# Optimization experiments

Measured on AMD Instinct MI355X. Metric: run time of the kernel, lower is better.

The kernel has to match this reference:

```python
import jax, jax.numpy as jnp
import numpy as np

N_HEADS = 16


def setup_inputs() -> dict:
    key = jax.random.key(0)
    ks = jax.random.split(key, 5)
    B, T, C = 4, 2048, 1024
    scale = 0.02
    return {
        "x": jax.random.normal(ks[0], (B, T, C), dtype=jnp.float32),
        "w_attn": jax.random.normal(ks[1], (C, 3 * C), dtype=jnp.float32) * scale,
        "b_attn": jax.random.normal(ks[2], (3 * C,), dtype=jnp.float32) * scale,
        "w_proj": jax.random.normal(ks[3], (C, C), dtype=jnp.float32) * scale,
        "b_proj": jax.random.normal(ks[4], (C,), dtype=jnp.float32) * scale,
    }


def reference(x, w_attn, b_attn, w_proj, b_proj):
    B, T, C = x.shape
    H = N_HEADS
    D = C // H  # head dim
    qkv = x @ w_attn + b_attn  # [B,T,3C]
    q, k, v = jnp.split(qkv, 3, axis=-1)
    # [B,T,C] -> [B,H,T,D]
    q = q.reshape(B, T, H, D).transpose(0, 2, 1, 3)
    k = k.reshape(B, T, H, D).transpose(0, 2, 1, 3)
    v = v.reshape(B, T, H, D).transpose(0, 2, 1, 3)
    att = jnp.einsum("bhtd,bhsd->bhts", q, k) * (1.0 / jnp.sqrt(jnp.float32(D)))
    causal = jnp.tril(jnp.ones((T, T), dtype=bool))  # [T,T]
    att = jnp.where(causal[None, None], att, -jnp.inf)
    att = jax.nn.softmax(att, axis=-1)
    y = jnp.einsum("bhts,bhsd->bhtd", att, v)  # [B,H,T,D]
    y = y.transpose(0, 2, 1, 3).reshape(B, T, C)
    return y @ w_proj + b_proj
```

## Files before the change

### kernel.cpp

```cpp
#include <hip/hip_runtime.h>
#include <hip/hip_bf16.h>
#include <math.h>

typedef __attribute__((ext_vector_type(8))) short short8;
typedef __attribute__((ext_vector_type(4))) short short4v;
typedef __attribute__((ext_vector_type(4))) float f32x4;
typedef __attribute__((ext_vector_type(2))) unsigned int uint2v;
typedef unsigned int u32;

#define MFMA16(a, b, c) __builtin_amdgcn_mfma_f32_16x16x16bf16_1k(a, b, c, 0, 0, 0)
#define MFMA32(a, b, c) __builtin_amdgcn_mfma_f32_16x16x32_bf16(a, b, c, 0, 0, 0)

#define GLB(p) ((const __attribute__((address_space(1))) u32*)(p))
#define LDS(p) ((__attribute__((address_space(3))) u32*)(p))

#define QSCALE 0.18033688011111204f

#define KV_STRIDE 72
#define KV_TILE 4608
#define KV_CHUNK 9216

__device__ __forceinline__ unsigned short f2bf(float f) {
  unsigned int u = __float_as_uint(f);
  u += 0x7fffu + ((u >> 16) & 1u);
  return (unsigned short)(u >> 16);
}


__global__ __launch_bounds__(256) void cvt_bf16(const float* __restrict__ in,
                                                unsigned short* __restrict__ out, int n4) {
  int i = blockIdx.x * blockDim.x + threadIdx.x;
  if (i < n4) {
    float4 f = ((const float4*)in)[i];
    ushort4 o;
    o.x = f2bf(f.x); o.y = f2bf(f.y); o.z = f2bf(f.z); o.w = f2bf(f.w);
    ((ushort4*)out)[i] = o;
  }
}

__global__ __launch_bounds__(256) void transpose_cvt(const float* __restrict__ in,
                                                     unsigned short* __restrict__ out,
                                                     int R, int C) {
  __shared__ float tile[32][33];
  int bx = blockIdx.x * 32;
  int by = blockIdx.y * 32;
  int tx = threadIdx.x, ty = threadIdx.y;
#pragma unroll
  for (int i = 0; i < 32; i += 8)
    tile[ty + i][tx] = in[(size_t)(by + ty + i) * C + bx + tx];
  __syncthreads();
#pragma unroll
  for (int i = 0; i < 32; i += 8)
    out[(size_t)(bx + ty + i) * R + by + tx] = f2bf(tile[tx][ty + i]);
}


template <int MODE>
__global__ __launch_bounds__(256)
void gemm_bt(const unsigned short* __restrict__ A, const unsigned short* __restrict__ Bt,
             const float* __restrict__ bias, float* __restrict__ outf,
             unsigned short* __restrict__ q_ws, unsigned short* __restrict__ kv_ws,
             int M, int N, int K) {
  __shared__ unsigned short As[128 * 32];
  __shared__ unsigned short Bs[128 * 32];
  const int tid = threadIdx.x;
  const int wid = tid >> 6;
  const int lane = tid & 63;
  const int quad = lane >> 4;
  const int l15 = lane & 15;
  const int m0 = blockIdx.x * 128;
  const int n0 = blockIdx.y * 128;
  const int wm = (wid >> 1) * 64;
  const int wn = (wid & 1) * 64;

  const int srow = wid * 32 + (lane >> 2);
  const int scol = (lane & 3) * 8;
  const unsigned short* ga0 = A + (size_t)(m0 + srow) * K + scol;
  const unsigned short* ga1 = ga0 + (size_t)16 * K;
  const unsigned short* gb0 = Bt + (size_t)(n0 + srow) * K + scol;
  const unsigned short* gb1 = gb0 + (size_t)16 * K;
  unsigned short* la0 = As + srow * 32 + scol;
  unsigned short* la1 = la0 + 16 * 32;
  unsigned short* lb0 = Bs + srow * 32 + scol;
  unsigned short* lb1 = lb0 + 16 * 32;

  f32x4 acc[4][4];
#pragma unroll
  for (int i = 0; i < 4; i++)
#pragma unroll
    for (int j = 0; j < 4; j++) acc[i][j] = (f32x4){0.f, 0.f, 0.f, 0.f};

  for (int k0 = 0; k0 < K; k0 += 32) {
    __builtin_amdgcn_global_load_lds(GLB(ga0 + k0), LDS(la0), 16, 0, 0);
    __builtin_amdgcn_global_load_lds(GLB(ga1 + k0), LDS(la1), 16, 0, 0);
    __builtin_amdgcn_global_load_lds(GLB(gb0 + k0), LDS(lb0), 16, 0, 0);
    __builtin_amdgcn_global_load_lds(GLB(gb1 + k0), LDS(lb1), 16, 0, 0);
    __syncthreads();
    short8 af[4], bf[4];
#pragma unroll
    for (int i = 0; i < 4; i++)
      af[i] = *(const short8*)(As + (wm + i * 16 + l15) * 32 + quad * 8);
#pragma unroll
    for (int j = 0; j < 4; j++)
      bf[j] = *(const short8*)(Bs + (wn + j * 16 + l15) * 32 + quad * 8);
#pragma unroll
    for (int i = 0; i < 4; i++)
#pragma unroll
      for (int j = 0; j < 4; j++)
        acc[i][j] = MFMA32(af[i], bf[j], acc[i][j]);
    __syncthreads();
  }

  const int colbase = n0 + wn;
  const int which = colbase >> 10;

  if (MODE == 0 && which == 2) {
    short4v idf;
#pragma unroll
    for (int j4 = 0; j4 < 4; j4++) idf[j4] = (quad * 4 + j4 == l15) ? (short)0x3F80 : (short)0;
    const int cb = colbase & 1023;
    const int h = cb >> 6;
#pragma unroll
    for (int j = 0; j < 4; j++) {
      const float bv = bias[colbase + j * 16 + l15];
      const int d0 = (cb & 63) + j * 16 + quad * 4;
#pragma unroll
      for (int i = 0; i < 4; i++) {
        short4v pf;
#pragma unroll
        for (int r = 0; r < 4; r++) pf[r] = (short)f2bf(acc[i][j][r] + bv);
        f32x4 dt = MFMA16(pf, idf, ((f32x4){0.f, 0.f, 0.f, 0.f}));
        const int t = m0 + wm + i * 16 + l15;
        const int b = t >> 11;
        const int tt = t & 2047;
        const size_t cbase =
            ((size_t)((b * 16 + h) * 32) + (tt >> 6)) * KV_CHUNK + KV_TILE;
        const int tl = tt & 63;
#pragma unroll
        for (int r = 0; r < 4; r++)
          kv_ws[cbase + (size_t)(d0 + r) * KV_STRIDE + tl] = f2bf(dt[r]);
      }
    }
  } else {
#pragma unroll
    for (int j = 0; j < 4; j++) {
      const int col = colbase + j * 16 + l15;
      const float bv = bias[col];
#pragma unroll
      for (int i = 0; i < 4; i++) {
#pragma unroll
        for (int r = 0; r < 4; r++) {
          const int row = m0 + wm + i * 16 + quad * 4 + r;
          float v = acc[i][j][r] + bv;
          if (MODE == 0) {
            const int c = col & 1023;
            const int h = c >> 6;
            const int d = c & 63;
            const int b = row >> 11;
            const int t = row & 2047;
            if (which == 0) {
              q_ws[(((size_t)(b * 16 + h) * 2048 + t) * 64) + d] = f2bf(v * QSCALE);
            } else {
              const size_t cbase = ((size_t)((b * 16 + h) * 32) + (t >> 6)) * KV_CHUNK;
              kv_ws[cbase + (size_t)(t & 63) * KV_STRIDE + d] = f2bf(v);
            }
          } else {
            outf[(size_t)row * N + col] = v;
          }
        }
      }
    }
  }
}


__global__ __launch_bounds__(256, 4)
void attn_fwd(const unsigned short* __restrict__ q_ws, const unsigned short* __restrict__ kv_ws,
              unsigned short* __restrict__ y_ws) {
  __shared__ unsigned short KV[2][KV_CHUNK];
  const int tid = threadIdx.x;
  const int w = tid >> 6;
  const int lane = tid & 63;
  const int quad = lane >> 4;
  const int l15 = lane & 15;
  const int ip = blockIdx.x;
  const int bh = blockIdx.y;
  const unsigned short* Qp = q_ws + (size_t)bh * 2048 * 64;
  const unsigned short* KVp = kv_ws + (size_t)bh * 32 * KV_CHUNK;

  const int qA = ip * 64 + w * 16;
  const int qB = (31 - ip) * 64 + w * 16;

  short8 qfr[2][2];
#pragma unroll
  for (int c = 0; c < 2; c++) {
    qfr[0][c] = *(const short8*)(Qp + (size_t)(qA + l15) * 64 + c * 32 + quad * 8);
    qfr[1][c] = *(const short8*)(Qp + (size_t)(qB + l15) * 64 + c * 32 + quad * 8);
  }

  f32x4 o[2][4];
#pragma unroll
  for (int f = 0; f < 2; f++)
#pragma unroll
    for (int db = 0; db < 4; db++) o[f][db] = (f32x4){0.f, 0.f, 0.f, 0.f};
  float lsum[2] = {0.f, 0.f};

  const int nch = 32 - ip;

  for (int i = w; i < 18; i += 4)
    __builtin_amdgcn_global_load_lds(GLB(KVp + i * 512 + lane * 8),
                                     LDS(&KV[0][i * 512 + lane * 8]), 16, 0, 0);

  for (int c = 0; c < nch; c++) {
    __syncthreads();
    const int buf = c & 1;
    if (c + 1 < nch) {
      const unsigned short* src = KVp + (size_t)(c + 1) * KV_CHUNK;
      for (int i = w; i < 18; i += 4)
        __builtin_amdgcn_global_load_lds(GLB(src + i * 512 + lane * 8),
                                         LDS(&KV[buf ^ 1][i * 512 + lane * 8]), 16, 0, 0);
    }
    const unsigned short* Ksb = KV[buf];
    const unsigned short* Vtb = KV[buf] + KV_TILE;
    const int kbase = c * 64;

#pragma unroll
    for (int tb = 0; tb < 2; tb++) {
      const int kb = kbase + tb * 32;
      if (kb > qB + 15) break;
      const int kloc = tb * 32;
      short8 kf[2][2];
#pragma unroll
      for (int t2 = 0; t2 < 2; t2++)
#pragma unroll
        for (int cc = 0; cc < 2; cc++)
          kf[t2][cc] =
              *(const short8*)(&Ksb[(kloc + t2 * 16 + l15) * KV_STRIDE + cc * 32 + quad * 8]);
      short4v vf[2][4];
#pragma unroll
      for (int t2 = 0; t2 < 2; t2++)
#pragma unroll
        for (int db = 0; db < 4; db++)
          vf[t2][db] =
              *(const short4v*)(&Vtb[(db * 16 + l15) * KV_STRIDE + kloc + t2 * 16 + quad * 4]);

#pragma unroll
      for (int f = 0; f < 2; f++) {
        const int qf0 = f ? qB : qA;
        if (kb > qf0 + 15) continue;
        f32x4 s0 = (f32x4){0.f, 0.f, 0.f, 0.f};
        f32x4 s1 = (f32x4){0.f, 0.f, 0.f, 0.f};
        s0 = MFMA32(kf[0][0], qfr[f][0], s0);
        s0 = MFMA32(kf[0][1], qfr[f][1], s0);
        s1 = MFMA32(kf[1][0], qfr[f][0], s1);
        s1 = MFMA32(kf[1][1], qfr[f][1], s1);
        const int qg = qf0 + l15;
        if (kb + 31 > qf0) {
#pragma unroll
          for (int r = 0; r < 4; r++) {
            if (kb + quad * 4 + r > qg) s0[r] = -INFINITY;
            if (kb + 16 + quad * 4 + r > qg) s1[r] = -INFINITY;
          }
        }
        float p[8];
#pragma unroll
        for (int r = 0; r < 4; r++) {
          p[r] = __builtin_amdgcn_exp2f(s0[r]);
          p[4 + r] = __builtin_amdgcn_exp2f(s1[r]);
        }
        lsum[f] += ((p[0] + p[1]) + (p[2] + p[3])) + ((p[4] + p[5]) + (p[6] + p[7]));
        u32 u[8];
#pragma unroll
        for (int i = 0; i < 8; i++) u[i] = __float_as_uint(p[i]) + 0x8000u;
        uint2v t0, t1;
        t0.x = __builtin_amdgcn_perm(u[1], u[0], 0x07060302u);
        t0.y = __builtin_amdgcn_perm(u[3], u[2], 0x07060302u);
        t1.x = __builtin_amdgcn_perm(u[5], u[4], 0x07060302u);
        t1.y = __builtin_amdgcn_perm(u[7], u[6], 0x07060302u);
        short4v pf0 = __builtin_bit_cast(short4v, t0);
        short4v pf1 = __builtin_bit_cast(short4v, t1);
#pragma unroll
        for (int db = 0; db < 4; db++) {
          o[f][db] = MFMA16(vf[0][db], pf0, o[f][db]);
          o[f][db] = MFMA16(vf[1][db], pf1, o[f][db]);
        }
      }
    }
  }

  const int b = bh >> 4, h = bh & 15;
#pragma unroll
  for (int f = 0; f < 2; f++) {
    float ls = lsum[f];
    ls += __shfl_xor(ls, 16);
    ls += __shfl_xor(ls, 32);
    const int qg = (f ? qB : qA) + l15;
    const float inv = 1.0f / ls;
    const size_t rowoff = ((size_t)(b * 2048 + qg)) * 1024 + h * 64;
#pragma unroll
    for (int db = 0; db < 4; db++) {
      ushort4 ov;
      ov.x = f2bf(o[f][db][0] * inv);
      ov.y = f2bf(o[f][db][1] * inv);
      ov.z = f2bf(o[f][db][2] * inv);
      ov.w = f2bf(o[f][db][3] * inv);
      *(ushort4*)(y_ws + rowoff + db * 16 + quad * 4) = ov;
    }
  }
}


extern "C" void kernel_launch(void* const* d_in, const int* in_sizes, int n_in,
                              void* d_out, int out_size, void* d_ws, size_t ws_size,
                              hipStream_t stream) {
  const float* x = (const float*)d_in[0];
  const float* w_attn = (const float*)d_in[1];
  const float* b_attn = (const float*)d_in[2];
  const float* w_proj = (const float*)d_in[3];
  const float* b_proj = (const float*)d_in[4];
  float* out = (float*)d_out;

  unsigned short* xb = (unsigned short*)d_ws;
  unsigned short* wat = xb + (size_t)8192 * 1024;
  unsigned short* wpt = wat + (size_t)3072 * 1024;
  unsigned short* q_ws = wpt + (size_t)1024 * 1024;
  unsigned short* kv_ws = q_ws + (size_t)8388608;
  unsigned short* y_ws = xb;

  cvt_bf16<<<8192, 256, 0, stream>>>(x, xb, 2097152);
  transpose_cvt<<<dim3(96, 32), dim3(32, 8), 0, stream>>>(w_attn, wat, 1024, 3072);
  transpose_cvt<<<dim3(32, 32), dim3(32, 8), 0, stream>>>(w_proj, wpt, 1024, 1024);

  gemm_bt<0><<<dim3(64, 24), 256, 0, stream>>>(xb, wat, b_attn, nullptr, q_ws, kv_ws,
                                               8192, 3072, 1024);
  attn_fwd<<<dim3(16, 64), 256, 0, stream>>>(q_ws, kv_ws, y_ws);
  gemm_bt<1><<<dim3(64, 8), 256, 0, stream>>>(y_ws, wpt, b_proj, out, nullptr, nullptr,
                                              8192, 1024, 1024);
}
```

Before: 272.6 us.

## Process four query tiles per attention block and vectorize QKV epilogue stores

Each attention block now handles four balanced query tiles (ip, 15-ip, 16+ip, 31-ip) instead of two, halving the grid. Each KV chunk staged in LDS is therefore reused by twice as many query fragments, which cuts global and LDS loading per unit of work. The cost is more accumulator registers per thread, the removal of the occupancy hint from the launch bounds, and fewer blocks to spread across CUs. Separately, the QKV GEMM epilogue writes Q and K through the MFMA identity-transpose trick and writes V directly, all as 4-wide ushort4 stores instead of scalar stores.

```diff
diff --git a/kernel.cpp b/kernel.cpp
--- a/kernel.cpp
+++ b/kernel.cpp
@@ -114,31 +114,62 @@
   const int colbase = n0 + wn;
   const int which = colbase >> 10;
 
-  if (MODE == 0 && which == 2) {
-    short4v idf;
-#pragma unroll
-    for (int j4 = 0; j4 < 4; j4++) idf[j4] = (quad * 4 + j4 == l15) ? (short)0x3F80 : (short)0;
-    const int cb = colbase & 1023;
-    const int h = cb >> 6;
-#pragma unroll
-    for (int j = 0; j < 4; j++) {
-      const float bv = bias[colbase + j * 16 + l15];
-      const int d0 = (cb & 63) + j * 16 + quad * 4;
-#pragma unroll
-      for (int i = 0; i < 4; i++) {
-        short4v pf;
-#pragma unroll
-        for (int r = 0; r < 4; r++) pf[r] = (short)f2bf(acc[i][j][r] + bv);
-        f32x4 dt = MFMA16(pf, idf, ((f32x4){0.f, 0.f, 0.f, 0.f}));
-        const int t = m0 + wm + i * 16 + l15;
-        const int b = t >> 11;
-        const int tt = t & 2047;
-        const size_t cbase =
-            ((size_t)((b * 16 + h) * 32) + (tt >> 6)) * KV_CHUNK + KV_TILE;
-        const int tl = tt & 63;
-#pragma unroll
-        for (int r = 0; r < 4; r++)
-          kv_ws[cbase + (size_t)(d0 + r) * KV_STRIDE + tl] = f2bf(dt[r]);
+  if (MODE == 0) {
+    const int h = (colbase & 1023) >> 6;
+    if (which == 2) {
+#pragma unroll
+      for (int j = 0; j < 4; j++) {
+        const float bv = bias[colbase + j * 16 + l15];
+        const int d = j * 16 + l15;
+#pragma unroll
+        for (int i = 0; i < 4; i++) {
+          const int t = m0 + wm + i * 16 + quad * 4;
+          const int b = t >> 11;
+          const int tt = t & 2047;
+          ushort4 pv;
+          pv.x = f2bf(acc[i][j][0] + bv);
+          pv.y = f2bf(acc[i][j][1] + bv);
+          pv.z = f2bf(acc[i][j][2] + bv);
+          pv.w = f2bf(acc[i][j][3] + bv);
+          const size_t cbase = ((size_t)((b * 16 + h) * 32) + (tt >> 6)) * KV_CHUNK + KV_TILE;
+          *(ushort4*)(&kv_ws[cbase + (size_t)d * KV_STRIDE + (tt & 63)]) = pv;
+        }
+      }
+    } else {
+      short4v idf;
+#pragma unroll
+      for (int j4 = 0; j4 < 4; j4++)
+        idf[j4] = (quad * 4 + j4 == l15) ? (short)0x3F80 : (short)0;
+#pragma unroll
+      for (int j = 0; j < 4; j++) {
+        const float bv = bias[colbase + j * 16 + l15];
+#pragma unroll
+        for (int i = 0; i < 4; i++) {
+          short4v pf;
+          if (which == 0) {
+#pragma unroll
+            for (int r = 0; r < 4; r++) pf[r] = (short)f2bf((acc[i][j][r] + bv) * QSCALE);
+          } else {
+#pragma unroll
+            for (int r = 0; r < 4; r++) pf[r] = (short)f2bf(acc[i][j][r] + bv);
+          }
+          f32x4 dt = MFMA16(pf, idf, ((f32x4){0.f, 0.f, 0.f, 0.f}));
+          const int t = m0 + wm + i * 16 + l15;
+          const int b = t >> 11;
+          const int tt = t & 2047;
+          const int dd = j * 16 + quad * 4;
+          ushort4 qv;
+          qv.x = f2bf(dt[0]);
+          qv.y = f2bf(dt[1]);
+          qv.z = f2bf(dt[2]);
+          qv.w = f2bf(dt[3]);
+          if (which == 0) {
+            *(ushort4*)(&q_ws[(((size_t)((b * 16 + h) * 2048) + tt) * 64) + dd]) = qv;
+          } else {
+            const size_t cbase = ((size_t)((b * 16 + h) * 32) + (tt >> 6)) * KV_CHUNK;
+            *(ushort4*)(&kv_ws[cbase + (size_t)(tt & 63) * KV_STRIDE + dd]) = qv;
+          }
+        }
       }
     }
   } else {
@@ -151,22 +182,7 @@
 #pragma unroll
         for (int r = 0; r < 4; r++) {
           const int row = m0 + wm + i * 16 + quad * 4 + r;
-          float v = acc[i][j][r] + bv;
-          if (MODE == 0) {
-            const int c = col & 1023;
-            const int h = c >> 6;
-            const int d = c & 63;
-            const int b = row >> 11;
-            const int t = row & 2047;
-            if (which == 0) {
-              q_ws[(((size_t)(b * 16 + h) * 2048 + t) * 64) + d] = f2bf(v * QSCALE);
-            } else {
-              const size_t cbase = ((size_t)((b * 16 + h) * 32) + (t >> 6)) * KV_CHUNK;
-              kv_ws[cbase + (size_t)(t & 63) * KV_STRIDE + d] = f2bf(v);
-            }
-          } else {
-            outf[(size_t)row * N + col] = v;
-          }
+          outf[(size_t)row * N + col] = acc[i][j][r] + bv;
         }
       }
     }
@@ -174,7 +190,7 @@
 }
 
 
-__global__ __launch_bounds__(256, 4)
+__global__ __launch_bounds__(256)
 void attn_fwd(const unsigned short* __restrict__ q_ws, const unsigned short* __restrict__ kv_ws,
               unsigned short* __restrict__ y_ws) {
   __shared__ unsigned short KV[2][KV_CHUNK];
@@ -188,22 +204,25 @@
   const unsigned short* Qp = q_ws + (size_t)bh * 2048 * 64;
   const unsigned short* KVp = kv_ws + (size_t)bh * 32 * KV_CHUNK;
 
-  const int qA = ip * 64 + w * 16;
-  const int qB = (31 - ip) * 64 + w * 16;
-
-  short8 qfr[2][2];
-#pragma unroll
-  for (int c = 0; c < 2; c++) {
-    qfr[0][c] = *(const short8*)(Qp + (size_t)(qA + l15) * 64 + c * 32 + quad * 8);
-    qfr[1][c] = *(const short8*)(Qp + (size_t)(qB + l15) * 64 + c * 32 + quad * 8);
-  }
-
-  f32x4 o[2][4];
-#pragma unroll
-  for (int f = 0; f < 2; f++)
+  int qT[4];
+  qT[0] = ip * 64 + w * 16;
+  qT[1] = (15 - ip) * 64 + w * 16;
+  qT[2] = (16 + ip) * 64 + w * 16;
+  qT[3] = (31 - ip) * 64 + w * 16;
+
+  short8 qfr[4][2];
+#pragma unroll
+  for (int f = 0; f < 4; f++)
+#pragma unroll
+    for (int c = 0; c < 2; c++)
+      qfr[f][c] = *(const short8*)(Qp + (size_t)(qT[f] + l15) * 64 + c * 32 + quad * 8);
+
+  f32x4 o[4][4];
+#pragma unroll
+  for (int f = 0; f < 4; f++)
 #pragma unroll
     for (int db = 0; db < 4; db++) o[f][db] = (f32x4){0.f, 0.f, 0.f, 0.f};
-  float lsum[2] = {0.f, 0.f};
+  float lsum[4] = {0.f, 0.f, 0.f, 0.f};
 
   const int nch = 32 - ip;
 
@@ -227,7 +246,7 @@
 #pragma unroll
     for (int tb = 0; tb < 2; tb++) {
       const int kb = kbase + tb * 32;
-      if (kb > qB + 15) break;
+      if (kb > qT[3] + 15) break;
       const int kloc = tb * 32;
       short8 kf[2][2];
 #pragma unroll
@@ -245,8 +264,8 @@
               *(const short4v*)(&Vtb[(db * 16 + l15) * KV_STRIDE + kloc + t2 * 16 + quad * 4]);
 
 #pragma unroll
-      for (int f = 0; f < 2; f++) {
-        const int qf0 = f ? qB : qA;
+      for (int f = 0; f < 4; f++) {
+        const int qf0 = qT[f];
         if (kb > qf0 + 15) continue;
         f32x4 s0 = (f32x4){0.f, 0.f, 0.f, 0.f};
         f32x4 s1 = (f32x4){0.f, 0.f, 0.f, 0.f};
@@ -290,11 +309,11 @@
 
   const int b = bh >> 4, h = bh & 15;
 #pragma unroll
-  for (int f = 0; f < 2; f++) {
+  for (int f = 0; f < 4; f++) {
     float ls = lsum[f];
     ls += __shfl_xor(ls, 16);
     ls += __shfl_xor(ls, 32);
-    const int qg = (f ? qB : qA) + l15;
+    const int qg = qT[f] + l15;
     const float inv = 1.0f / ls;
     const size_t rowoff = ((size_t)(b * 2048 + qg)) * 1024 + h * 64;
 #pragma unroll
@@ -333,7 +352,7 @@
 
   gemm_bt<0><<<dim3(64, 24), 256, 0, stream>>>(xb, wat, b_attn, nullptr, q_ws, kv_ws,
                                                8192, 3072, 1024);
-  attn_fwd<<<dim3(16, 64), 256, 0, stream>>>(q_ws, kv_ws, y_ws);
+  attn_fwd<<<dim3(8, 64), 256, 0, stream>>>(q_ws, kv_ws, y_ws);
   gemm_bt<1><<<dim3(64, 8), 256, 0, stream>>>(y_ws, wpt, b_proj, out, nullptr, nullptr,
                                               8192, 1024, 1024);
 }
```

Result: faster. 266.1 us (-2.4%).
